# Kernel optimization log

Hardware: AMD Instinct MI355X
Metric: run time of the kernel (lower is better)

## Reference

```python
import jax, jax.numpy as jnp
import numpy as np

N = 100000      # nodes
E = 1600000     # edges (avg degree 16)
D_IN = 256
H = 128         # hidden_dim
D_OUT = 64
BN_EPS = 1e-5


def setup_inputs() -> dict:
    key = jax.random.key(0)
    ks = jax.random.split(key, 16)
    s = 0.05  # small init scale
    x = jax.random.normal(ks[0], (N, D_IN), jnp.float32)
    edge_index = jax.random.randint(ks[1], (2, E), 0, N)
    inp = {
        "x": x,
        "edge_index": edge_index,
        "w_in": jax.random.normal(ks[2], (D_IN, H), jnp.float32) * s,
        "b_in": jnp.zeros((H,), jnp.float32),
        # SAGEConv layer 1: lin_l (neighbors, with bias) + lin_r (self, no bias)
        "w_l1": jax.random.normal(ks[3], (H, H), jnp.float32) * s,
        "b_l1": jnp.zeros((H,), jnp.float32),
        "w_r1": jax.random.normal(ks[4], (H, H), jnp.float32) * s,
        "g1": jnp.ones((H,), jnp.float32),
        "be1": jnp.zeros((H,), jnp.float32),
        # SAGEConv layer 2
        "w_l2": jax.random.normal(ks[5], (H, H), jnp.float32) * s,
        "b_l2": jnp.zeros((H,), jnp.float32),
        "w_r2": jax.random.normal(ks[6], (H, H), jnp.float32) * s,
        "g2": jnp.ones((H,), jnp.float32),
        "be2": jnp.zeros((H,), jnp.float32),
        "w_out": jax.random.normal(ks[7], (H, D_OUT), jnp.float32) * s,
        "b_out": jnp.zeros((D_OUT,), jnp.float32),
    }
    return inp


def _sage_conv(x, src, dst, w_l, b_l, w_r):
    # gather messages from source nodes, mean-aggregate at target nodes
    msgs = x[src]                                           # [E, H]
    agg = jax.ops.segment_sum(msgs, dst, num_segments=N)    # [N, H]
    deg = jax.ops.segment_sum(jnp.ones((src.shape[0], 1), x.dtype), dst,
                              num_segments=N)               # [N, 1]
    mean = agg / jnp.maximum(deg, 1.0)
    return mean @ w_l + b_l + x @ w_r


def _bn_eval(h, gamma, beta):
    # BatchNorm1d in eval mode: running_mean=0, running_var=1
    return h * (gamma / jnp.sqrt(1.0 + BN_EPS)) + beta


def reference(x, edge_index, w_in, b_in,
              w_l1, b_l1, w_r1, g1, be1,
              w_l2, b_l2, w_r2, g2, be2,
              w_out, b_out):
    src, dst = edge_index[0], edge_index[1]
    h = jax.nn.relu(x @ w_in + b_in)                         # [N, H]
    h = _sage_conv(h, src, dst, w_l1, b_l1, w_r1)
    h = jax.nn.relu(_bn_eval(h, g1, be1))                    # dropout off (eval)
    h = _sage_conv(h, src, dst, w_l2, b_l2, w_r2)
    h = jax.nn.relu(_bn_eval(h, g2, be2))
    return h @ w_out + b_out                                 # [N, D_OUT]
```

## Files before the change

kernel.cpp:

```cpp
#include <hip/hip_runtime.h>

#define DIN 256
#define H   128
#define DOUT 64

#define EPI_RELU 0
#define EPI_BN   1
#define EPI_NONE 2

#define BKT_SHIFT 7
#define BKT_NODES 128
#define BKT_CAP   4096
#define CSR_CAP   4608

typedef __attribute__((ext_vector_type(8))) short bf16x8;
typedef __attribute__((ext_vector_type(4))) float f32x4;

__device__ inline unsigned short f2bf(float f) {
  union { float f; unsigned u; } v; v.f = f;
  unsigned u = v.u;
  u += 0x7FFFu + ((u >> 16) & 1u);
  return (unsigned short)(u >> 16);
}
__device__ inline float bf2f(unsigned u16) {
  union { unsigned u; float f; } v; v.u = u16 << 16;
  return v.f;
}

#define FILL_TPB 1024
#define FILL_EPT 16
#define FILL_EPB (FILL_TPB * FILL_EPT)

__global__ __launch_bounds__(FILL_TPB) void bucket_fill(
    const int* __restrict__ src, const int* __restrict__ dst,
    int* __restrict__ bcur, unsigned* __restrict__ bedges,
    int nbkt, int e) {
  __shared__ int hist[1024];
  int tid = threadIdx.x;
  int base = blockIdx.x * FILL_EPB;
  for (int i = tid; i < nbkt; i += FILL_TPB) hist[i] = 0;
  __syncthreads();

  int es[FILL_EPT], ed[FILL_EPT];
#pragma unroll
  for (int j = 0; j < FILL_EPT; ++j) {
    int i = base + j * FILL_TPB + tid;
    if (i < e) {
      es[j] = src[i];
      ed[j] = dst[i];
      atomicAdd(&hist[ed[j] >> BKT_SHIFT], 1);
    } else {
      es[j] = -1; ed[j] = 0;
    }
  }
  __syncthreads();
  for (int b = tid; b < nbkt; b += FILL_TPB) {
    int cnt = hist[b];
    hist[b] = cnt ? atomicAdd(&bcur[b], cnt) : 0;
  }
  __syncthreads();
#pragma unroll
  for (int j = 0; j < FILL_EPT; ++j) {
    if (es[j] >= 0) {
      int b = ed[j] >> BKT_SHIFT;
      int p = atomicAdd(&hist[b], 1);
      if (p < BKT_CAP)
        bedges[(size_t)b * BKT_CAP + p] =
            (unsigned)es[j] | ((unsigned)(ed[j] & (BKT_NODES - 1)) << 17);
    }
  }
}

__global__ __launch_bounds__(256) void bucket_sort(
    const int* __restrict__ bcur, const unsigned* __restrict__ bedges,
    int* __restrict__ csr, int2* __restrict__ rowdeg, int n) {
  __shared__ unsigned rec[BKT_CAP];
  __shared__ int srcs[CSR_CAP];
  __shared__ int hist[BKT_NODES];
  __shared__ int cursor[BKT_NODES];
  __shared__ int s_total;
  int tid = threadIdx.x;
  int b = blockIdx.x;
  int cnt = bcur[b];
  if (cnt > BKT_CAP) cnt = BKT_CAP;
  const unsigned* eb = bedges + (size_t)b * BKT_CAP;

  if (tid < BKT_NODES) hist[tid] = 0;
  __syncthreads();
  for (int i = tid; i < cnt; i += 256) {
    unsigned r = eb[i];
    rec[i] = r;
    atomicAdd(&hist[(r >> 17) & 127], 1);
  }
  __syncthreads();
  int myc = (tid < BKT_NODES) ? hist[tid] : 0;
  int myc4 = (myc + 3) & ~3;
  if (tid < BKT_NODES) hist[tid] = myc4;
  __syncthreads();
#pragma unroll
  for (int off = 1; off < BKT_NODES; off <<= 1) {
    int v = 0;
    if (tid < BKT_NODES && tid >= off) v = hist[tid - off];
    __syncthreads();
    if (tid < BKT_NODES) hist[tid] += v;
    __syncthreads();
  }
  int start = 0;
  if (tid < BKT_NODES) {
    start = hist[tid] - myc4;
    cursor[tid] = start;
    int node = b * BKT_NODES + tid;
    if (node < n) rowdeg[node] = make_int2(b * CSR_CAP + start, myc);
    if (tid == BKT_NODES - 1) s_total = hist[tid];
  }
  __syncthreads();
  for (int i = tid; i < cnt; i += 256) {
    unsigned r = rec[i];
    int p = atomicAdd(&cursor[(r >> 17) & 127], 1);
    srcs[p] = (int)(r & 0x1FFFFu);
  }
  if (tid < BKT_NODES) {
    for (int g = start + myc; g < start + myc4; ++g) srcs[g] = 0;
  }
  __syncthreads();
  int total = s_total;
  if (tid < 16 && total + tid < CSR_CAP) srcs[total + tid] = 0;
  __syncthreads();
  int tot16 = total + 16;
  if (tot16 > CSR_CAP) tot16 = CSR_CAP;
  for (int i = tid; i < tot16; i += 256)
    csr[(size_t)b * CSR_CAP + i] = srcs[i];
}

__global__ __launch_bounds__(256) void agg_kernel(
    const unsigned* __restrict__ h, const int2* __restrict__ rowdeg,
    const int* __restrict__ csr, unsigned* __restrict__ mean, int n) {
  int wid = (blockIdx.x * 256 + threadIdx.x) >> 6;
  int lane = threadIdx.x & 63;
  int grp = lane >> 4;
  int c = lane & 15;
  int node = wid * 4 + grp;
  bool valid = node < n;
  if (!valid) node = 0;
  int2 rd = rowdeg[node];
  int beg = rd.x, d = rd.y;

  const uint4* hv = (const uint4*)h;
  float a[8];
#pragma unroll
  for (int k = 0; k < 8; ++k) a[k] = 0.f;

  for (int j0 = 0; j0 < d; j0 += 16) {
    int rem = d - j0;
    const int4* sp = (const int4*)(csr + beg + j0);
    int sv[16];
    *(int4*)&sv[0]  = sp[0];
    *(int4*)&sv[4]  = sp[1];
    *(int4*)&sv[8]  = sp[2];
    *(int4*)&sv[12] = sp[3];
#pragma unroll
    for (int jj = 0; jj < 16; ++jj) {
      float w = (jj < rem) ? 1.f : 0.f;
      uint4 v = hv[(unsigned)(sv[jj] * 16 + c)];
#pragma unroll
      for (int k = 0; k < 4; ++k) {
        unsigned u = ((const unsigned*)&v)[k];
        union { unsigned u; float f; } lo, hi;
        lo.u = u << 16;
        hi.u = u & 0xffff0000u;
        a[2 * k]     = fmaf(w, lo.f, a[2 * k]);
        a[2 * k + 1] = fmaf(w, hi.f, a[2 * k + 1]);
      }
    }
  }

  if (valid) {
    float invd = 1.f / (float)(d > 0 ? d : 1);
    uint4 o;
    o.x = (unsigned)f2bf(a[0] * invd) | ((unsigned)f2bf(a[1] * invd) << 16);
    o.y = (unsigned)f2bf(a[2] * invd) | ((unsigned)f2bf(a[3] * invd) << 16);
    o.z = (unsigned)f2bf(a[4] * invd) | ((unsigned)f2bf(a[5] * invd) << 16);
    o.w = (unsigned)f2bf(a[6] * invd) | ((unsigned)f2bf(a[7] * invd) << 16);
    ((uint4*)mean)[(unsigned)(node * 16 + c)] = o;
  }
}

__global__ __launch_bounds__(256) void prep_w(
    const float* __restrict__ w_in, const float* __restrict__ w_l1,
    const float* __restrict__ w_r1, const float* __restrict__ w_l2,
    const float* __restrict__ w_r2, const float* __restrict__ w_out,
    unsigned short* __restrict__ t_in, unsigned short* __restrict__ t_l1,
    unsigned short* __restrict__ t_r1, unsigned short* __restrict__ t_l2,
    unsigned short* __restrict__ t_r2, unsigned short* __restrict__ t_out) {
  int i = blockIdx.x * 256 + threadIdx.x;
  const float* s; unsigned short* d; int K, M, off;
  if (i < 32768)       { s = w_in;  d = t_in;  K = 256; M = 128; off = i; }
  else if (i < 49152)  { s = w_l1;  d = t_l1;  K = 128; M = 128; off = i - 32768; }
  else if (i < 65536)  { s = w_r1;  d = t_r1;  K = 128; M = 128; off = i - 49152; }
  else if (i < 81920)  { s = w_l2;  d = t_l2;  K = 128; M = 128; off = i - 65536; }
  else if (i < 98304)  { s = w_r2;  d = t_r2;  K = 128; M = 128; off = i - 81920; }
  else if (i < 106496) { s = w_out; d = t_out; K = 128; M = 64;  off = i - 98304; }
  else return;
  int m = off / K, k = off % K;
  d[off] = f2bf(s[(size_t)k * M + m]);
}

template <int NPH, int KOFF2, int AKA, int AKW, int M, int EPI, bool AFP32, bool OUTF32>
__global__ __launch_bounds__(256) void gemm_mfma(
    const void* __restrict__ A1, const void* __restrict__ A2,
    const unsigned short* __restrict__ W1, const unsigned short* __restrict__ W2,
    const float* __restrict__ bias, const float* __restrict__ gamma,
    const float* __restrict__ beta, void* __restrict__ Cv, int n) {
  constexpr int NT = M / 16;
  __shared__ __align__(16) unsigned short As[64 * 128];
  __shared__ __align__(16) unsigned short Bs[M * 128];

  int tid = threadIdx.x, lane = tid & 63, wave = tid >> 6;
  int m16 = lane & 15, quad = lane >> 4;
  int row0 = blockIdx.x * 64;
  int sr = lane >> 4;
  int sc = lane & 15;

  f32x4 acc[NT];
#pragma unroll
  for (int t = 0; t < NT; ++t) acc[t] = (f32x4){0.f, 0.f, 0.f, 0.f};

#pragma unroll
  for (int ph = 0; ph < NPH; ++ph) {
    const void* A_ = ph ? A2 : A1;
    const unsigned short* W = ph ? W2 : W1;
    const int koff = ph ? KOFF2 : 0;
    if (ph) __syncthreads();

    if constexpr (!AFP32) {
#pragma unroll
      for (int g = 0; g < 4; ++g) {
        int lr = wave * 16 + g * 4 + sr;
        int grow = row0 + lr; if (grow >= n) grow = n - 1;
        uint4 v = *(const uint4*)((const unsigned short*)A_ +
                                  (size_t)grow * AKA + koff + sc * 8);
        *(uint4*)&As[lr * 128 + ((sc + lr) & 15) * 8] = v;
      }
    } else {
      int sr2 = lane >> 5;
      int c32 = lane & 31;
#pragma unroll
      for (int g = 0; g < 8; ++g) {
        int lr = wave * 16 + g * 2 + sr2;
        int grow = row0 + lr; if (grow >= n) grow = n - 1;
        float4 v = *(const float4*)((const float*)A_ +
                                    (size_t)grow * AKA + koff + c32 * 4);
        unsigned p0 = (unsigned)f2bf(v.x) | ((unsigned)f2bf(v.y) << 16);
        unsigned p1 = (unsigned)f2bf(v.z) | ((unsigned)f2bf(v.w) << 16);
        int ch = c32 >> 1;
        *(uint2*)&As[lr * 128 + ((ch + lr) & 15) * 8 + (c32 & 1) * 4] =
            make_uint2(p0, p1);
      }
    }
#pragma unroll
    for (int g = 0; g < M / 16; ++g) {
      int br = wave * (M / 4) + g * 4 + sr;
      uint4 v = *(const uint4*)(W + (size_t)br * AKW + koff + sc * 8);
      *(uint4*)&Bs[br * 128 + ((sc + br) & 15) * 8] = v;
    }
    __syncthreads();

    int lrme = wave * 16 + m16;
#pragma unroll
    for (int kt = 0; kt < 4; ++kt) {
      int ch = kt * 4 + quad;
      bf16x8 a = *(const bf16x8*)&As[lrme * 128 + ((ch + lrme) & 15) * 8];
#pragma unroll
      for (int t = 0; t < NT; ++t) {
        int brow = t * 16 + m16;
        bf16x8 b = *(const bf16x8*)&Bs[brow * 128 + ((ch + brow) & 15) * 8];
        acc[t] = __builtin_amdgcn_mfma_f32_16x16x32_bf16(a, b, acc[t], 0, 0, 0);
      }
    }
  }

  const float inv_std = rsqrtf(1.f + 1e-5f);
#pragma unroll
  for (int t = 0; t < NT; ++t) {
    int col = t * 16 + m16;
    float bv = bias[col];
    float sc2 = 1.f, bt2 = 0.f;
    if constexpr (EPI == EPI_BN) {
      sc2 = gamma[col] * inv_std;
      bt2 = beta[col];
    }
#pragma unroll
    for (int r = 0; r < 4; ++r) {
      int row = row0 + wave * 16 + quad * 4 + r;
      if (row < n) {
        float v = acc[t][r] + bv;
        if constexpr (EPI == EPI_BN) v = fmaxf(v * sc2 + bt2, 0.f);
        else if constexpr (EPI == EPI_RELU) v = fmaxf(v, 0.f);
        if constexpr (OUTF32)
          ((float*)Cv)[(size_t)row * M + col] = v;
        else
          ((unsigned short*)Cv)[(size_t)row * M + col] = f2bf(v);
      }
    }
  }
}

extern "C" void kernel_launch(void* const* d_in, const int* in_sizes, int n_in,
                              void* d_out, int out_size, void* d_ws, size_t ws_size,
                              hipStream_t stream) {
  const float* x     = (const float*)d_in[0];
  const int*   ei    = (const int*)d_in[1];
  const float* w_in  = (const float*)d_in[2];
  const float* b_in  = (const float*)d_in[3];
  const float* w_l1  = (const float*)d_in[4];
  const float* b_l1  = (const float*)d_in[5];
  const float* w_r1  = (const float*)d_in[6];
  const float* g1    = (const float*)d_in[7];
  const float* be1   = (const float*)d_in[8];
  const float* w_l2  = (const float*)d_in[9];
  const float* b_l2  = (const float*)d_in[10];
  const float* w_r2  = (const float*)d_in[11];
  const float* g2    = (const float*)d_in[12];
  const float* be2   = (const float*)d_in[13];
  const float* w_out = (const float*)d_in[14];
  const float* b_out = (const float*)d_in[15];
  float* out = (float*)d_out;

  int N = in_sizes[0] / DIN;
  int E = in_sizes[1] / 2;
  const int* src = ei;
  const int* dst = ei + E;
  int nbkt = (N + BKT_NODES - 1) / BKT_NODES;

  char* ws = (char*)d_ws;
  size_t off = 0;
  auto alloc = [&](size_t bytes) -> char* {
    char* p = ws + off;
    off += (bytes + 255) & ~(size_t)255;
    return p;
  };
  unsigned short* buf0 = (unsigned short*)alloc((size_t)N * H * 2);
  unsigned short* buf1 = (unsigned short*)alloc((size_t)N * H * 2);
  unsigned short* buf2 = (unsigned short*)alloc((size_t)N * H * 2);
  int* bcur        = (int*)alloc((size_t)nbkt * 4);
  unsigned* bedges = (unsigned*)alloc((size_t)nbkt * BKT_CAP * 4);
  int* csr         = (int*)alloc((size_t)nbkt * CSR_CAP * 4);
  int2* rowdeg     = (int2*)alloc((size_t)N * 8);
  unsigned short* t_in  = (unsigned short*)alloc(32768 * 2);
  unsigned short* t_l1  = (unsigned short*)alloc(16384 * 2);
  unsigned short* t_r1  = (unsigned short*)alloc(16384 * 2);
  unsigned short* t_l2  = (unsigned short*)alloc(16384 * 2);
  unsigned short* t_r2  = (unsigned short*)alloc(16384 * 2);
  unsigned short* t_out = (unsigned short*)alloc(8192 * 2);
  (void)ws_size;

  hipMemsetAsync(bcur, 0, (size_t)nbkt * 4, stream);
  bucket_fill<<<(E + FILL_EPB - 1) / FILL_EPB, FILL_TPB, 0, stream>>>(
      src, dst, bcur, bedges, nbkt, E);
  bucket_sort<<<nbkt, 256, 0, stream>>>(bcur, bedges, csr, rowdeg, N);
  prep_w<<<(106496 + 255) / 256, 256, 0, stream>>>(
      w_in, w_l1, w_r1, w_l2, w_r2, w_out, t_in, t_l1, t_r1, t_l2, t_r2, t_out);

  int gblocks = (N + 63) / 64;
  int ablocks = (N + 15) / 16;

  gemm_mfma<2, 128, 256, 256, 128, EPI_RELU, true, false><<<gblocks, 256, 0, stream>>>(
      x, x, t_in, t_in, b_in, nullptr, nullptr, buf0, N);
  agg_kernel<<<ablocks, 256, 0, stream>>>((const unsigned*)buf0, rowdeg,
                                          csr, (unsigned*)buf1, N);
  gemm_mfma<2, 0, 128, 128, 128, EPI_BN, false, false><<<gblocks, 256, 0, stream>>>(
      buf1, buf0, t_l1, t_r1, b_l1, g1, be1, buf2, N);
  agg_kernel<<<ablocks, 256, 0, stream>>>((const unsigned*)buf2, rowdeg,
                                          csr, (unsigned*)buf0, N);
  gemm_mfma<2, 0, 128, 128, 128, EPI_BN, false, false><<<gblocks, 256, 0, stream>>>(
      buf0, buf2, t_l2, t_r2, b_l2, g2, be2, buf1, N);
  gemm_mfma<1, 0, 128, 128, 64, EPI_NONE, false, true><<<gblocks, 256, 0, stream>>>(
      buf1, buf1, t_out, t_out, b_out, nullptr, nullptr, out, N);
}
```

Measured before the change: 425.7 us.

## Load A fragments directly to registers and stage B via global_load_lds

The GEMM kernel no longer stages the A tile through shared memory. Each lane now loads its MFMA A fragment straight from global memory into registers, converting fp32 to bf16 inline where needed. The weight tile B is copied into LDS with the direct global-to-LDS load builtin, using a swizzled source column so the LDS layout matches the old XOR-style swizzle. This is meant to cut LDS traffic, LDS capacity (raising occupancy) and VGPR round-trips, at the cost of less coalesced per-lane A global reads.

```diff
diff --git a/kernel.cpp b/kernel.cpp
--- a/kernel.cpp
+++ b/kernel.cpp
@@ -25,6 +25,15 @@
 __device__ inline float bf2f(unsigned u16) {
   union { unsigned u; float f; } v; v.u = u16 << 16;
   return v.f;
+}
+__device__ inline unsigned pk_bf16(float lo, float hi) {
+  return (unsigned)f2bf(lo) | ((unsigned)f2bf(hi) << 16);
+}
+
+__device__ inline void gload_lds16(const void* g, void* l) {
+  __builtin_amdgcn_global_load_lds(
+      (const __attribute__((address_space(1))) void*)g,
+      (__attribute__((address_space(3))) void*)l, 16, 0, 0);
 }
 
 #define FILL_TPB 1024
@@ -177,10 +186,10 @@
   if (valid) {
     float invd = 1.f / (float)(d > 0 ? d : 1);
     uint4 o;
-    o.x = (unsigned)f2bf(a[0] * invd) | ((unsigned)f2bf(a[1] * invd) << 16);
-    o.y = (unsigned)f2bf(a[2] * invd) | ((unsigned)f2bf(a[3] * invd) << 16);
-    o.z = (unsigned)f2bf(a[4] * invd) | ((unsigned)f2bf(a[5] * invd) << 16);
-    o.w = (unsigned)f2bf(a[6] * invd) | ((unsigned)f2bf(a[7] * invd) << 16);
+    o.x = pk_bf16(a[0] * invd, a[1] * invd);
+    o.y = pk_bf16(a[2] * invd, a[3] * invd);
+    o.z = pk_bf16(a[4] * invd, a[5] * invd);
+    o.w = pk_bf16(a[6] * invd, a[7] * invd);
     ((uint4*)mean)[(unsigned)(node * 16 + c)] = o;
   }
 }
@@ -212,7 +221,6 @@
     const float* __restrict__ bias, const float* __restrict__ gamma,
     const float* __restrict__ beta, void* __restrict__ Cv, int n) {
   constexpr int NT = M / 16;
-  __shared__ __align__(16) unsigned short As[64 * 128];
   __shared__ __align__(16) unsigned short Bs[M * 128];
 
   int tid = threadIdx.x, lane = tid & 63, wave = tid >> 6;
@@ -221,6 +229,9 @@
   int sr = lane >> 4;
   int sc = lane & 15;
 
+  int arow = row0 + wave * 16 + m16;
+  if (arow >= n) arow = n - 1;
+
   f32x4 acc[NT];
 #pragma unroll
   for (int t = 0; t < NT; ++t) acc[t] = (f32x4){0.f, 0.f, 0.f, 0.f};
@@ -232,49 +243,45 @@
     const int koff = ph ? KOFF2 : 0;
     if (ph) __syncthreads();
 
-    if constexpr (!AFP32) {
-#pragma unroll
-      for (int g = 0; g < 4; ++g) {
-        int lr = wave * 16 + g * 4 + sr;
-        int grow = row0 + lr; if (grow >= n) grow = n - 1;
-        uint4 v = *(const uint4*)((const unsigned short*)A_ +
-                                  (size_t)grow * AKA + koff + sc * 8);
-        *(uint4*)&As[lr * 128 + ((sc + lr) & 15) * 8] = v;
-      }
-    } else {
-      int sr2 = lane >> 5;
-      int c32 = lane & 31;
-#pragma unroll
-      for (int g = 0; g < 8; ++g) {
-        int lr = wave * 16 + g * 2 + sr2;
-        int grow = row0 + lr; if (grow >= n) grow = n - 1;
-        float4 v = *(const float4*)((const float*)A_ +
-                                    (size_t)grow * AKA + koff + c32 * 4);
-        unsigned p0 = (unsigned)f2bf(v.x) | ((unsigned)f2bf(v.y) << 16);
-        unsigned p1 = (unsigned)f2bf(v.z) | ((unsigned)f2bf(v.w) << 16);
-        int ch = c32 >> 1;
-        *(uint2*)&As[lr * 128 + ((ch + lr) & 15) * 8 + (c32 & 1) * 4] =
-            make_uint2(p0, p1);
-      }
-    }
 #pragma unroll
     for (int g = 0; g < M / 16; ++g) {
       int br = wave * (M / 4) + g * 4 + sr;
-      uint4 v = *(const uint4*)(W + (size_t)br * AKW + koff + sc * 8);
-      *(uint4*)&Bs[br * 128 + ((sc + br) & 15) * 8] = v;
+      int cs = (sc - br) & 15;
+      gload_lds16(W + (size_t)br * AKW + koff + cs * 8,
+                  &Bs[(wave * (M / 4) + g * 4) * 128]);
+    }
+
+    bf16x8 afrag[4];
+    if constexpr (!AFP32) {
+      const unsigned short* Ab =
+          (const unsigned short*)A_ + (size_t)arow * AKA + koff;
+#pragma unroll
+      for (int kt = 0; kt < 4; ++kt)
+        afrag[kt] = *(const bf16x8*)(Ab + (kt * 4 + quad) * 8);
+    } else {
+      const float* Af = (const float*)A_ + (size_t)arow * AKA + koff;
+#pragma unroll
+      for (int kt = 0; kt < 4; ++kt) {
+        float4 v0 = *(const float4*)(Af + (kt * 4 + quad) * 8);
+        float4 v1 = *(const float4*)(Af + (kt * 4 + quad) * 8 + 4);
+        union { unsigned u[4]; bf16x8 v; } pk;
+        pk.u[0] = pk_bf16(v0.x, v0.y);
+        pk.u[1] = pk_bf16(v0.z, v0.w);
+        pk.u[2] = pk_bf16(v1.x, v1.y);
+        pk.u[3] = pk_bf16(v1.z, v1.w);
+        afrag[kt] = pk.v;
+      }
     }
     __syncthreads();
 
-    int lrme = wave * 16 + m16;
 #pragma unroll
     for (int kt = 0; kt < 4; ++kt) {
       int ch = kt * 4 + quad;
-      bf16x8 a = *(const bf16x8*)&As[lrme * 128 + ((ch + lrme) & 15) * 8];
 #pragma unroll
       for (int t = 0; t < NT; ++t) {
         int brow = t * 16 + m16;
         bf16x8 b = *(const bf16x8*)&Bs[brow * 128 + ((ch + brow) & 15) * 8];
-        acc[t] = __builtin_amdgcn_mfma_f32_16x16x32_bf16(a, b, acc[t], 0, 0, 0);
+        acc[t] = __builtin_amdgcn_mfma_f32_16x16x32_bf16(afrag[kt], b, acc[t], 0, 0, 0);
       }
     }
   }
```

Result: no change. 420.4 us (-1.2%).
